# Performance work log

Hardware: AMD Instinct MI355X
Metric: run time of the kernel (lower is better)

Reference implementation:

```python
import jax, jax.numpy as jnp
import numpy as np


def setup_inputs() -> dict:
    key = jax.random.key(0)
    k1, k2, k3 = jax.random.split(key, 3)
    B, T, C, H, W = 4, 1024, 64, 8, 8
    E = C * H * W  # 4096 == embed_dim
    x = jax.random.normal(k1, (B, T, C, H, W), dtype=jnp.float32)
    Wqkv = jax.random.normal(k2, (E, 3 * E), dtype=jnp.float32) * (E ** -0.5)
    Wout = jax.random.normal(k3, (E, E), dtype=jnp.float32) * (E ** -0.5)
    bout = jnp.zeros((E,), dtype=jnp.float32)
    return {"x": x, "Wqkv": Wqkv, "Wout": Wout, "bout": bout}


def reference(x, Wqkv, Wout, bout):
    B, T, C, H, W = x.shape
    E = C * H * W
    heads = 8
    dh = E // heads
    # NOTE: original scales by embed_dim**-0.5, NOT head_dim**-0.5
    scale = E ** -0.5

    xf = x.reshape(B, T, E)                      # [B,T,E]
    qkv = xf @ Wqkv                              # [B,T,3E]
    q, k, v = jnp.split(qkv, 3, axis=-1)
    q = q.reshape(B, T, heads, dh)
    k = k.reshape(B, T, heads, dh)
    v = v.reshape(B, T, heads, dh)

    scores = jnp.einsum('bthd,bshd->bhts', q, k) * scale  # [B,h,T,T]
    attn = jax.nn.softmax(scores, axis=-1)
    out = jnp.einsum('bhts,bshd->bthd', attn, v)           # [B,T,h,dh]
    out = out.reshape(B, T, E) @ Wout + bout               # [B,T,E]
    return out.reshape(B, T, C, H, W)
```

## Files before the change

### kernel.cpp

```cpp
#include <hip/hip_runtime.h>
#include <hip/hip_bf16.h>

typedef __attribute__((ext_vector_type(8))) __bf16 bf16x8;
typedef __attribute__((ext_vector_type(4))) __bf16 bf16x4;
typedef __attribute__((ext_vector_type(4))) float f32x4;
typedef __attribute__((ext_vector_type(4))) int i32x4;

#define MFMA16(a, b, c) __builtin_amdgcn_mfma_f32_16x16x32_bf16((a), (b), (c), 0, 0, 0)
#define MFMAI8(a, b, c) __builtin_amdgcn_mfma_i32_16x16x64_i8((a), (b), (c), 0, 0, 0)

__global__ __launch_bounds__(256) void k_quantX(const float* __restrict__ x,
                                                __bf16* __restrict__ xb,
                                                char* __restrict__ xi8,
                                                float* __restrict__ sa) {
  int row = blockIdx.x, tid = threadIdx.x;
  const float* src = x + (size_t)row * 4096 + tid * 16;
  float arr[16];
#pragma unroll
  for (int j = 0; j < 4; ++j) {
    float4 v = ((const float4*)src)[j];
    arr[j * 4 + 0] = v.x; arr[j * 4 + 1] = v.y;
    arr[j * 4 + 2] = v.z; arr[j * 4 + 3] = v.w;
  }
  float m = 0.f;
#pragma unroll
  for (int e = 0; e < 16; ++e) m = fmaxf(m, fabsf(arr[e]));
#pragma unroll
  for (int off = 32; off; off >>= 1) m = fmaxf(m, __shfl_xor(m, off, 64));
  __shared__ float wmx[4];
  if ((tid & 63) == 0) wmx[tid >> 6] = m;
  __syncthreads();
  m = fmaxf(fmaxf(wmx[0], wmx[1]), fmaxf(wmx[2], wmx[3]));
  m = fmaxf(m, 1e-20f);
  float inv = 127.f / m;
  __bf16* db = xb + (size_t)row * 4096 + tid * 16;
#pragma unroll
  for (int j = 0; j < 2; ++j) {
    bf16x8 o;
#pragma unroll
    for (int e = 0; e < 8; ++e) o[e] = (__bf16)arr[j * 8 + e];
    *(bf16x8*)(db + j * 8) = o;
  }
  int pk[4];
#pragma unroll
  for (int j = 0; j < 4; ++j) {
    int w = 0;
#pragma unroll
    for (int e = 0; e < 4; ++e) {
      int q = (int)__builtin_rintf(arr[j * 4 + e] * inv);
      q = q < -127 ? -127 : (q > 127 ? 127 : q);
      w |= (q & 255) << (e * 8);
    }
    pk[j] = w;
  }
  int4 pv; pv.x = pk[0]; pv.y = pk[1]; pv.z = pk[2]; pv.w = pk[3];
  *(int4*)(xi8 + (size_t)row * 4096 + tid * 16) = pv;
  if (tid == 0) sa[row] = m / 127.f;
}

__global__ __launch_bounds__(256) void k_quantW(const __bf16* __restrict__ wT,
                                                char* __restrict__ wi8,
                                                float* __restrict__ sb) {
  int row = blockIdx.x, tid = threadIdx.x;
  const __bf16* src = wT + (size_t)row * 4096 + tid * 16;
  float arr[16];
#pragma unroll
  for (int j = 0; j < 2; ++j) {
    bf16x8 v = *(const bf16x8*)(src + j * 8);
#pragma unroll
    for (int e = 0; e < 8; ++e) arr[j * 8 + e] = (float)v[e];
  }
  float m = 0.f;
#pragma unroll
  for (int e = 0; e < 16; ++e) m = fmaxf(m, fabsf(arr[e]));
#pragma unroll
  for (int off = 32; off; off >>= 1) m = fmaxf(m, __shfl_xor(m, off, 64));
  __shared__ float wmx[4];
  if ((tid & 63) == 0) wmx[tid >> 6] = m;
  __syncthreads();
  m = fmaxf(fmaxf(wmx[0], wmx[1]), fmaxf(wmx[2], wmx[3]));
  m = fmaxf(m, 1e-20f);
  float inv = 127.f / m;
  int pk[4];
#pragma unroll
  for (int j = 0; j < 4; ++j) {
    int w = 0;
#pragma unroll
    for (int e = 0; e < 4; ++e) {
      int q = (int)__builtin_rintf(arr[j * 4 + e] * inv);
      q = q < -127 ? -127 : (q > 127 ? 127 : q);
      w |= (q & 255) << (e * 8);
    }
    pk[j] = w;
  }
  int4 pv; pv.x = pk[0]; pv.y = pk[1]; pv.z = pk[2]; pv.w = pk[3];
  *(int4*)(wi8 + (size_t)row * 4096 + tid * 16) = pv;
  if (tid == 0) sb[row] = m / 127.f;
}

__global__ __launch_bounds__(256) void k_prep(const float* __restrict__ Wqkv,
                                              __bf16* __restrict__ wT) {
  __shared__ float tl[64][68];
  int id = blockIdx.x, tid = threadIdx.x;
  int c0 = (id % 192) * 64, r0 = (id / 192) * 64;
  const int R = 4096, C = 12288;
#pragma unroll
  for (int j = 0; j < 4; ++j) {
    int idx = j * 256 + tid;
    int row = idx >> 4, q4 = (idx & 15) * 4;
    float4 v = *(const float4*)(Wqkv + (size_t)(r0 + row) * C + c0 + q4);
    tl[row][q4 + 0] = v.x; tl[row][q4 + 1] = v.y;
    tl[row][q4 + 2] = v.z; tl[row][q4 + 3] = v.w;
  }
  __syncthreads();
#pragma unroll
  for (int j = 0; j < 2; ++j) {
    int idx = j * 256 + tid;
    int orow = idx >> 3, ch = (idx & 7) * 8;
    bf16x8 pk;
#pragma unroll
    for (int e = 0; e < 8; ++e) pk[e] = (__bf16)tl[ch + e][orow];
    *(bf16x8*)(wT + (size_t)(c0 + orow) * R + r0 + ch) = pk;
  }
}

__global__ __launch_bounds__(256) void k_post1(const __bf16* __restrict__ qkv,
                                               __bf16* __restrict__ vt,
                                               const float* __restrict__ Wout,
                                               __bf16* __restrict__ woT) {
  __shared__ float tlf[64][68];
  __shared__ __bf16 tlh[64][72];
  int id = blockIdx.x, tid = threadIdx.x;
  if (id < 4096) {
    int bx = id & 7, by = (id >> 3) & 15, p = id >> 7;
    int b = p >> 3, h = p & 7;
    int d0 = bx * 64, s0 = by * 64;
    const __bf16* src = qkv + (size_t)b * 1024 * 12288 + 8192 + h * 512;
#pragma unroll
    for (int j = 0; j < 2; ++j) {
      int idx = j * 256 + tid;
      int row = idx >> 3, ch = (idx & 7) * 8;
      bf16x8 v = *(const bf16x8*)(src + (size_t)(s0 + row) * 12288 + d0 + ch);
#pragma unroll
      for (int e = 0; e < 8; ++e) tlh[row][ch + e] = v[e];
    }
    __syncthreads();
#pragma unroll
    for (int j = 0; j < 2; ++j) {
      int idx = j * 256 + tid;
      int orow = idx >> 3, ch = (idx & 7) * 8;
      bf16x8 pk;
#pragma unroll
      for (int e = 0; e < 8; ++e) pk[e] = tlh[ch + e][orow];
      *(bf16x8*)(vt + (size_t)p * 524288 + (size_t)(d0 + orow) * 1024 + s0 + ch) = pk;
    }
    return;
  }
  int t = id - 4096;
  int c0 = (t & 63) * 64, r0 = (t >> 6) * 64;
  const int R = 4096, C = 4096;
#pragma unroll
  for (int j = 0; j < 4; ++j) {
    int idx = j * 256 + tid;
    int row = idx >> 4, q4 = (idx & 15) * 4;
    float4 v = *(const float4*)(Wout + (size_t)(r0 + row) * C + c0 + q4);
    tlf[row][q4 + 0] = v.x; tlf[row][q4 + 1] = v.y;
    tlf[row][q4 + 2] = v.z; tlf[row][q4 + 3] = v.w;
  }
  __syncthreads();
#pragma unroll
  for (int j = 0; j < 2; ++j) {
    int idx = j * 256 + tid;
    int orow = idx >> 3, ch = (idx & 7) * 8;
    bf16x8 pk;
#pragma unroll
    for (int e = 0; e < 8; ++e) pk[e] = (__bf16)tlf[ch + e][orow];
    *(bf16x8*)(woT + (size_t)(c0 + orow) * R + r0 + ch) = pk;
  }
}

#define BARRIER() __builtin_amdgcn_s_barrier()
#define SCHED0() __builtin_amdgcn_sched_barrier(0)
#define VMC8() asm volatile("s_waitcnt vmcnt(8)" ::: "memory")
#define VMC4() asm volatile("s_waitcnt vmcnt(4)" ::: "memory")
#define LGKM(N)                                                   \
  do {                                                            \
    asm volatile("s_waitcnt lgkmcnt(" #N ")" ::: "memory");       \
    __builtin_amdgcn_sched_barrier(0);                            \
  } while (0)

#define LDA(AF, buf, mh)                                                      \
  do {                                                                        \
    _Pragma("unroll") for (int mi = 0; mi < 4; ++mi) {                        \
      int r = wm * 64 + mi * 16 + r16;                                        \
      _Pragma("unroll") for (int ks = 0; ks < 2; ++ks) {                      \
        int gg = ks * 4 + g;                                                  \
        AF[mi][ks] = *(const bf16x8*)(ldsB + (buf)*32768 + (mh)*16384 +       \
                                      r * 128 + ((gg ^ (r & 7)) << 4));       \
      }                                                                       \
    }                                                                         \
  } while (0)

#define LDB(BQ, buf, nh)                                                      \
  do {                                                                        \
    _Pragma("unroll") for (int ni = 0; ni < 2; ++ni) {                        \
      int r = wn * 32 + ni * 16 + r16;                                        \
      _Pragma("unroll") for (int ks = 0; ks < 2; ++ks) {                      \
        int gg = ks * 4 + g;                                                  \
        BQ[ni][ks] = *(const bf16x8*)(ldsB + 65536 + (buf)*32768 +            \
                                      (nh)*16384 + r * 128 +                  \
                                      ((gg ^ (r & 7)) << 4));                 \
      }                                                                       \
    }                                                                         \
  } while (0)

#define QUAD(AF, mh, nh, BQ)                                                  \
  do {                                                                        \
    __builtin_amdgcn_s_setprio(1);                                            \
    _Pragma("unroll") for (int ks = 0; ks < 2; ++ks)                          \
        _Pragma("unroll") for (int mi = 0; mi < 4; ++mi)                      \
            _Pragma("unroll") for (int ni = 0; ni < 2; ++ni)                  \
                acc[(mh)*4 + mi][(nh)*2 + ni] =                               \
                    MFMA16(AF[mi][ks], BQ[ni][ks],                            \
                           acc[(mh)*4 + mi][(nh)*2 + ni]);                    \
    __builtin_amdgcn_s_setprio(0);                                            \
    __builtin_amdgcn_sched_barrier(0);                                        \
  } while (0)

#define STAGE_A(mh, tau)                                                      \
  do {                                                                        \
    int tc = (tau) < NT ? (tau) : NT - 1;                                     \
    char* dbase = ldsB + ((tau)&1) * 32768 + (mh)*16384;                      \
    _Pragma("unroll") for (int i = 0; i < 2; ++i)                             \
        __builtin_amdgcn_global_load_lds(                                     \
            (const __attribute__((address_space(1))) void*)(Ap +              \
                offA[i][mh] + tc * 64),                                       \
            (__attribute__((address_space(3))) void*)(dbase +                 \
                (i * 512 + w * 64) * 16), 16, 0, 0);                          \
  } while (0)

#define STAGE_B(nh, tau)                                                      \
  do {                                                                        \
    int tc = (tau) < NT ? (tau) : NT - 1;                                     \
    char* dbase = ldsB + 65536 + ((tau)&1) * 32768 + (nh)*16384;              \
    _Pragma("unroll") for (int i = 0; i < 2; ++i)                             \
        __builtin_amdgcn_global_load_lds(                                     \
            (const __attribute__((address_space(1))) void*)(Bp +              \
                offB[i][nh] + tc * 64),                                       \
            (__attribute__((address_space(3))) void*)(dbase +                 \
                (i * 512 + w * 64) * 16), 16, 0, 0);                          \
  } while (0)

#define STAGE4(tau)                                                           \
  do {                                                                        \
    STAGE_A(0, tau); STAGE_B(0, tau); STAGE_B(1, tau); STAGE_A(1, tau);       \
  } while (0)

#define TILE_LOOP()                                                           \
  STAGE4(0);                                                                  \
  STAGE4(1);                                                                  \
  for (int t = 0; t < NT; ++t) {                                              \
    int buf = t & 1;                                                          \
    VMC8();                                                                   \
    BARRIER();                                                                \
    LDA(af, buf, 0);                                                          \
    LDB(bq0, buf, 0);                                                         \
    SCHED0();                                                                 \
    LDB(bq1, buf, 1);                                                         \
    SCHED0();                                                                 \
    LDA(af2, buf, 1);                                                         \
    LGKM(12);                                                                 \
    QUAD(af, 0, 0, bq0);                                                      \
    LGKM(8);                                                                  \
    QUAD(af, 0, 1, bq1);                                                      \
    LGKM(0);                                                                  \
    BARRIER();                                                                \
    STAGE4(t + 2);                                                            \
    QUAD(af2, 1, 1, bq1);                                                     \
    QUAD(af2, 1, 0, bq0);                                                     \
  }

#define SETUP_OFFSETS()                                                       \
  int offA[2][2], offB[2][2];                                                 \
  _Pragma("unroll") for (int i = 0; i < 2; ++i) {                             \
    int c = i * 512 + tid;                                                    \
    int r = c >> 3, slot = c & 7;                                             \
    int colsw = (slot ^ (r & 7)) << 3;                                        \
    _Pragma("unroll") for (int h = 0; h < 2; ++h) {                           \
      int RA = (r >> 6) * 128 + h * 64 + (r & 63);                            \
      int RB = (r >> 5) * 64 + h * 32 + (r & 31);                             \
      offA[i][h] = RA * lda + colsw;                                          \
      offB[i][h] = RB * ldb + colsw;                                          \
    }                                                                         \
  }

template <int MODE>
__global__ __launch_bounds__(512, 2) void k_gemm8(
    const __bf16* __restrict__ Abase, const __bf16* __restrict__ Bbase,
    void* __restrict__ Cout, const float* __restrict__ aux,
    int lda, int ldb, int N, int K) {
  __shared__ __align__(128) __bf16 lds[65536];
  char* ldsB = (char*)lds;
  int tid = threadIdx.x;
  int w = tid >> 6, lane = tid & 63;
  int r16 = lane & 15, g = lane >> 4;
  int wm = w >> 2, wn = w & 3;

  int bx, by, z = blockIdx.z;
  if (MODE <= 1) {
    int gx = gridDim.x, gy = gridDim.y;
    int RX = gx >> 2, RY = gy >> 1;
    int orig = blockIdx.y * gx + blockIdx.x;
    int xcd = orig & 7, idx = orig >> 3;
    int lbx = idx / RY, lby = idx - lbx * RY;
    bx = (xcd & 3) * RX + lbx;
    by = (xcd >> 2) * RY + lby;
  } else if (MODE == 2) {
    int i = blockIdx.z * 16 + blockIdx.y * 4 + blockIdx.x;
    z = (i & 7) | (((i >> 7) & 3) << 3);
    int qt = (i >> 3) & 15;
    by = qt >> 2; bx = qt & 3;
  } else {
    int i = blockIdx.z * 8 + blockIdx.y * 2 + blockIdx.x;
    z = (i & 7) | (((i >> 6) & 3) << 3);
    int qt = (i >> 3) & 7;
    by = qt >> 1; bx = qt & 1;
  }
  int m0 = by * 256, n0 = bx * 256;

  const __bf16 *Ap, *Bp;
  if (MODE == 2) {
    int b = z >> 3, h = z & 7;
    Ap = Abase + (size_t)b * 1024 * 12288 + h * 512;
    Bp = Abase + (size_t)b * 1024 * 12288 + 4096 + h * 512;
  } else if (MODE == 3) {
    Ap = Abase + (size_t)z * 1048576;
    Bp = Bbase + (size_t)z * 524288;
  } else {
    Ap = Abase; Bp = Bbase;
  }
  Ap += (size_t)m0 * lda;
  Bp += (size_t)n0 * ldb;
  SETUP_OFFSETS()

  int NT = K >> 6;
  f32x4 acc[8][4];
#pragma unroll
  for (int a = 0; a < 8; ++a)
#pragma unroll
    for (int bq = 0; bq < 4; ++bq) acc[a][bq] = f32x4{0.f, 0.f, 0.f, 0.f};
  bf16x8 af[4][2], af2[4][2], bq0[2][2], bq1[2][2];

  TILE_LOOP()

  if (MODE == 2) {
    asm volatile("s_waitcnt vmcnt(0)" ::: "memory");
    __syncthreads();
    float* Lbuf = (float*)ldsB;
#pragma unroll
    for (int mig = 0; mig < 8; ++mig) {
#pragma unroll
      for (int ii = 0; ii < 4; ++ii) {
        int row = m0 + wm * 128 + mig * 16 + g * 4 + ii;
        float s = 0.f;
#pragma unroll
        for (int nig = 0; nig < 4; ++nig) {
          int col = n0 + wn * 64 + nig * 16 + r16;
          float e = __expf(acc[mig][nig][ii] * 0.015625f);
          ((__bf16*)Cout)[(size_t)z * 1048576 + (size_t)row * 1024 + col] =
              (__bf16)e;
          s += e;
        }
        s += __shfl_xor(s, 1, 64);
        s += __shfl_xor(s, 2, 64);
        s += __shfl_xor(s, 4, 64);
        s += __shfl_xor(s, 8, 64);
        if (r16 == 0)
          Lbuf[(wm * 4 + wn) * 128 + mig * 16 + g * 4 + ii] = s;
      }
    }
    __syncthreads();
    if (tid < 256) {
      int wmi = tid >> 7, rl = tid & 127;
      const float* base = Lbuf + wmi * 512;
      float s = base[rl] + base[128 + rl] + base[256 + rl] + base[384 + rl];
      ((float*)aux)[z * 4096 + bx * 1024 + m0 + tid] = s;
    }
    return;
  }

#pragma unroll
  for (int mig = 0; mig < 8; ++mig) {
#pragma unroll
    for (int ii = 0; ii < 4; ++ii) {
      int row = m0 + wm * 128 + mig * 16 + g * 4 + ii;
      float lval = 0.f;
      if (MODE == 3)
        lval = aux[z * 4096 + row] + aux[z * 4096 + 1024 + row] +
               aux[z * 4096 + 2048 + row] + aux[z * 4096 + 3072 + row];
#pragma unroll
      for (int nig = 0; nig < 4; ++nig) {
        int col = n0 + wn * 64 + nig * 16 + r16;
        float v = acc[mig][nig][ii];
        if (MODE == 0) {
          ((__bf16*)Cout)[(size_t)row * N + col] = (__bf16)v;
        } else if (MODE == 1) {
          ((float*)Cout)[(size_t)row * N + col] = v + aux[col];
        } else if (MODE == 3) {
          ((__bf16*)Cout)[(size_t)((z >> 3) * 1024 + row) * 4096 +
                          (z & 7) * 512 + col] = (__bf16)(v / lval);
        }
      }
    }
  }
}

#define I8_SWZ(r) (((r) & 3) ^ (((r) >> 2) & 3))

#define I8_STAGE(tau)                                                         \
  do {                                                                        \
    int tc = (tau) < NT ? (tau) : NT - 1;                                     \
    char* da = ldsB + ((tau)&1) * 32768;                                      \
    _Pragma("unroll") for (int h = 0; h < 2; ++h) {                           \
      __builtin_amdgcn_global_load_lds(                                       \
          (const __attribute__((address_space(1))) void*)(Ap + offA[h] +      \
                                                          tc * 64),           \
          (__attribute__((address_space(3))) void*)(da + h * 8192 +           \
              w * 1024), 16, 0, 0);                                           \
      __builtin_amdgcn_global_load_lds(                                       \
          (const __attribute__((address_space(1))) void*)(Bp + offB[h] +      \
                                                          tc * 64),           \
          (__attribute__((address_space(3))) void*)(da + 16384 + h * 8192 +   \
              w * 1024), 16, 0, 0);                                           \
    }                                                                         \
  } while (0)

#define I8_QUAD(MIBASE)                                                       \
  do {                                                                        \
    __builtin_amdgcn_s_setprio(1);                                            \
    _Pragma("unroll") for (int mi = 0; mi < 4; ++mi)                          \
        _Pragma("unroll") for (int ni = 0; ni < 4; ++ni)                      \
            acc[(MIBASE) + mi][ni] = MFMAI8(af[mi], bq[ni],                   \
                                            acc[(MIBASE) + mi][ni]);          \
    __builtin_amdgcn_s_setprio(0);                                            \
    __builtin_amdgcn_sched_barrier(0);                                        \
  } while (0)

__global__ __launch_bounds__(512, 2) void k_gemm_i8(
    const char* __restrict__ Abase, const char* __restrict__ Bbase,
    __bf16* __restrict__ Cout, const float* __restrict__ sa,
    const float* __restrict__ sb) {
  __shared__ __align__(128) char ldsB[65536];
  const int lda = 4096, ldb = 4096, NT = 64;
  int tid = threadIdx.x;
  int w = tid >> 6, lane = tid & 63;
  int r16 = lane & 15, g = lane >> 4;
  int wm = w >> 2, wn = w & 3;

  int gx = gridDim.x, gy = gridDim.y;
  int RX = gx >> 2, RY = gy >> 1;
  int orig = blockIdx.y * gx + blockIdx.x;
  int xcd = orig & 7, idx = orig >> 3;
  int lbx = idx / RY, lby = idx - lbx * RY;
  int bx = (xcd & 3) * RX + lbx;
  int by = (xcd >> 2) * RY + lby;
  int m0 = by * 256, n0 = bx * 256;

  const char* Ap = Abase + (size_t)m0 * lda;
  const char* Bp = Bbase + (size_t)n0 * ldb;

  int offA[2], offB[2];
  {
    int rl = tid >> 2, slot = tid & 3;
    int slotg = (slot ^ I8_SWZ(rl)) << 4;
#pragma unroll
    for (int h = 0; h < 2; ++h) {
      offA[h] = (h * 128 + rl) * lda + slotg;
      offB[h] = (h * 128 + rl) * ldb + slotg;
    }
  }

  i32x4 acc[8][4];
#pragma unroll
  for (int a = 0; a < 8; ++a)
#pragma unroll
    for (int b = 0; b < 4; ++b) acc[a][b] = i32x4{0, 0, 0, 0};
  i32x4 af[4], af2[4], bq[4];

  I8_STAGE(0);
  I8_STAGE(1);
  for (int t = 0; t < NT; ++t) {
    int buf = t & 1;
    VMC4();
    BARRIER();
    {
      char* bbase = ldsB + buf * 32768 + 16384 + (wn >> 1) * 8192;
#pragma unroll
      for (int ni = 0; ni < 4; ++ni) {
        int rb = (wn & 1) * 64 + ni * 16 + r16;
        bq[ni] = *(const i32x4*)(bbase + rb * 64 + ((g ^ I8_SWZ(rb)) << 4));
      }
    }
    SCHED0();
    {
      char* abase = ldsB + buf * 32768 + wm * 8192;
#pragma unroll
      for (int mi = 0; mi < 4; ++mi) {
        int r = mi * 16 + r16;
        af[mi] = *(const i32x4*)(abase + r * 64 + ((g ^ I8_SWZ(r)) << 4));
      }
      SCHED0();
#pragma unroll
      for (int mi = 0; mi < 4; ++mi) {
        int r = 64 + mi * 16 + r16;
        af2[mi] = *(const i32x4*)(abase + r * 64 + ((g ^ I8_SWZ(r)) << 4));
      }
    }
    LGKM(4);
    I8_QUAD(0);
    LGKM(0);
    BARRIER();
    I8_STAGE(t + 2);
#pragma unroll
    for (int mi = 0; mi < 4; ++mi) af[mi] = af2[mi];
    I8_QUAD(4);
  }

#pragma unroll
  for (int mig = 0; mig < 8; ++mig) {
#pragma unroll
    for (int ii = 0; ii < 4; ++ii) {
      int row = m0 + wm * 128 + ((mig >> 2) * 64) + (mig & 3) * 16 + g * 4 + ii;
      float sav = sa[row];
#pragma unroll
      for (int nig = 0; nig < 4; ++nig) {
        int col = n0 + wn * 64 + nig * 16 + r16;
        float v = (float)acc[mig][nig][ii] * sav * sb[col];
        Cout[(size_t)row * 12288 + col] = (__bf16)v;
      }
    }
  }
}

extern "C" void kernel_launch(void* const* d_in, const int* in_sizes, int n_in,
                              void* d_out, int out_size, void* d_ws, size_t ws_size,
                              hipStream_t stream) {
  const float* x = (const float*)d_in[0];
  const float* Wqkv = (const float*)d_in[1];
  const float* Wout = (const float*)d_in[2];
  const float* bout = (const float*)d_in[3];
  float* out = (float*)d_out;
  char* ws = (char*)d_ws;

  __bf16* xb = (__bf16*)(ws);
  __bf16* wT = (__bf16*)(ws + 33554432);
  __bf16* P = (__bf16*)(ws + 33554432);
  __bf16* woT = (__bf16*)(ws + 33554432 + 67108864);
  __bf16* qkv = (__bf16*)(ws + 134217728);
  char* wi8 = (char*)(ws + 234881024);
  __bf16* vt = (__bf16*)(ws + 234881024);

  char* xi8 = (char*)d_out;
  float* sa = (float*)((char*)d_out + 16777216);
  float* sb = (float*)((char*)d_out + 16777216 + 65536);
  float* Lpart = (float*)((char*)d_out + 33554432);

  k_quantX<<<4096, 256, 0, stream>>>(x, xb, xi8, sa);
  k_prep<<<12288, 256, 0, stream>>>(Wqkv, wT);
  k_quantW<<<8192, 256, 0, stream>>>(wT, wi8, sb);
  k_gemm_i8<<<dim3(32, 16), 512, 0, stream>>>(xi8, wi8, qkv, sa, sb);
  k_gemm8<0><<<dim3(16, 16), 512, 0, stream>>>(
      xb, wT + (size_t)8192 * 4096, qkv + 8192, nullptr, 4096, 4096, 12288, 4096);
  k_post1<<<8192, 256, 0, stream>>>(qkv, vt, Wout, woT);
  k_gemm8<2><<<dim3(4, 4, 32), 512, 0, stream>>>(qkv, qkv, P, Lpart, 12288, 12288, 1024, 512);
  k_gemm8<3><<<dim3(2, 4, 32), 512, 0, stream>>>(P, vt, xb, Lpart, 1024, 1024, 512, 1024);
  k_gemm8<1><<<dim3(16, 16), 512, 0, stream>>>(xb, woT, out, bout, 4096, 4096, 4096, 4096);
}
```

Baseline: 584.5 us.

## Triple-buffer int8 GEMM LDS pipeline and merge quantX with weight transpose kernel

The int8 QKV GEMM goes from two LDS stages to three (96KB of LDS), prefetching two tiles ahead and waiting on vmcnt(8) instead of vmcnt(4), so global loads have more time to land. The x quantization kernel and the Wqkv transpose/convert kernel are merged into one launch that picks its path by block index, removing a launch boundary. The larger LDS footprint caps occupancy at one block per CU, and the merged kernel's shared tile also serves as the reduction scratch.

```diff
diff --git a/kernel.cpp b/kernel.cpp
--- a/kernel.cpp
+++ b/kernel.cpp
@@ -9,53 +9,81 @@
 #define MFMA16(a, b, c) __builtin_amdgcn_mfma_f32_16x16x32_bf16((a), (b), (c), 0, 0, 0)
 #define MFMAI8(a, b, c) __builtin_amdgcn_mfma_i32_16x16x64_i8((a), (b), (c), 0, 0, 0)
 
-__global__ __launch_bounds__(256) void k_quantX(const float* __restrict__ x,
-                                                __bf16* __restrict__ xb,
-                                                char* __restrict__ xi8,
-                                                float* __restrict__ sa) {
-  int row = blockIdx.x, tid = threadIdx.x;
-  const float* src = x + (size_t)row * 4096 + tid * 16;
-  float arr[16];
+__global__ __launch_bounds__(256) void k_prep(const float* __restrict__ x,
+                                              __bf16* __restrict__ xb,
+                                              char* __restrict__ xi8,
+                                              float* __restrict__ sa,
+                                              const float* __restrict__ Wqkv,
+                                              __bf16* __restrict__ wT) {
+  __shared__ float tl[64][68];
+  int id = blockIdx.x, tid = threadIdx.x;
+  if (id < 4096) {
+    int row = id;
+    const float* src = x + (size_t)row * 4096 + tid * 16;
+    float arr[16];
+#pragma unroll
+    for (int j = 0; j < 4; ++j) {
+      float4 v = ((const float4*)src)[j];
+      arr[j * 4 + 0] = v.x; arr[j * 4 + 1] = v.y;
+      arr[j * 4 + 2] = v.z; arr[j * 4 + 3] = v.w;
+    }
+    float m = 0.f;
+#pragma unroll
+    for (int e = 0; e < 16; ++e) m = fmaxf(m, fabsf(arr[e]));
+#pragma unroll
+    for (int off = 32; off; off >>= 1) m = fmaxf(m, __shfl_xor(m, off, 64));
+    float* wmx = &tl[0][0];
+    if ((tid & 63) == 0) wmx[tid >> 6] = m;
+    __syncthreads();
+    m = fmaxf(fmaxf(wmx[0], wmx[1]), fmaxf(wmx[2], wmx[3]));
+    m = fmaxf(m, 1e-20f);
+    float inv = 127.f / m;
+    __bf16* db = xb + (size_t)row * 4096 + tid * 16;
+#pragma unroll
+    for (int j = 0; j < 2; ++j) {
+      bf16x8 o;
+#pragma unroll
+      for (int e = 0; e < 8; ++e) o[e] = (__bf16)arr[j * 8 + e];
+      *(bf16x8*)(db + j * 8) = o;
+    }
+    int pk[4];
+#pragma unroll
+    for (int j = 0; j < 4; ++j) {
+      int wv = 0;
+#pragma unroll
+      for (int e = 0; e < 4; ++e) {
+        int q = (int)__builtin_rintf(arr[j * 4 + e] * inv);
+        q = q < -127 ? -127 : (q > 127 ? 127 : q);
+        wv |= (q & 255) << (e * 8);
+      }
+      pk[j] = wv;
+    }
+    int4 pv; pv.x = pk[0]; pv.y = pk[1]; pv.z = pk[2]; pv.w = pk[3];
+    *(int4*)(xi8 + (size_t)row * 4096 + tid * 16) = pv;
+    if (tid == 0) sa[row] = m / 127.f;
+    return;
+  }
+  int t = id - 4096;
+  int c0 = (t % 192) * 64, r0 = (t / 192) * 64;
+  const int R = 4096, C = 12288;
 #pragma unroll
   for (int j = 0; j < 4; ++j) {
-    float4 v = ((const float4*)src)[j];
-    arr[j * 4 + 0] = v.x; arr[j * 4 + 1] = v.y;
-    arr[j * 4 + 2] = v.z; arr[j * 4 + 3] = v.w;
-  }
-  float m = 0.f;
-#pragma unroll
-  for (int e = 0; e < 16; ++e) m = fmaxf(m, fabsf(arr[e]));
-#pragma unroll
-  for (int off = 32; off; off >>= 1) m = fmaxf(m, __shfl_xor(m, off, 64));
-  __shared__ float wmx[4];
-  if ((tid & 63) == 0) wmx[tid >> 6] = m;
+    int idx = j * 256 + tid;
+    int row = idx >> 4, q4 = (idx & 15) * 4;
+    float4 v = *(const float4*)(Wqkv + (size_t)(r0 + row) * C + c0 + q4);
+    tl[row][q4 + 0] = v.x; tl[row][q4 + 1] = v.y;
+    tl[row][q4 + 2] = v.z; tl[row][q4 + 3] = v.w;
+  }
   __syncthreads();
-  m = fmaxf(fmaxf(wmx[0], wmx[1]), fmaxf(wmx[2], wmx[3]));
-  m = fmaxf(m, 1e-20f);
-  float inv = 127.f / m;
-  __bf16* db = xb + (size_t)row * 4096 + tid * 16;
 #pragma unroll
   for (int j = 0; j < 2; ++j) {
-    bf16x8 o;
-#pragma unroll
-    for (int e = 0; e < 8; ++e) o[e] = (__bf16)arr[j * 8 + e];
-    *(bf16x8*)(db + j * 8) = o;
-  }
-  int pk[4];
-#pragma unroll
-  for (int j = 0; j < 4; ++j) {
-    int w = 0;
-#pragma unroll
-    for (int e = 0; e < 4; ++e) {
-      int q = (int)__builtin_rintf(arr[j * 4 + e] * inv);
-      q = q < -127 ? -127 : (q > 127 ? 127 : q);
-      w |= (q & 255) << (e * 8);
-    }
-    pk[j] = w;
-  }
-  int4 pv; pv.x = pk[0]; pv.y = pk[1]; pv.z = pk[2]; pv.w = pk[3];
-  *(int4*)(xi8 + (size_t)row * 4096 + tid * 16) = pv;
-  if (tid == 0) sa[row] = m / 127.f;
+    int idx = j * 256 + tid;
+    int orow = idx >> 3, ch = (idx & 7) * 8;
+    bf16x8 pk;
+#pragma unroll
+    for (int e = 0; e < 8; ++e) pk[e] = (__bf16)tl[ch + e][orow];
+    *(bf16x8*)(wT + (size_t)(c0 + orow) * R + r0 + ch) = pk;
+  }
 }
 
 __global__ __launch_bounds__(256) void k_quantW(const __bf16* __restrict__ wT,
@@ -96,32 +124,6 @@
   int4 pv; pv.x = pk[0]; pv.y = pk[1]; pv.z = pk[2]; pv.w = pk[3];
   *(int4*)(wi8 + (size_t)row * 4096 + tid * 16) = pv;
   if (tid == 0) sb[row] = m / 127.f;
-}
-
-__global__ __launch_bounds__(256) void k_prep(const float* __restrict__ Wqkv,
-                                              __bf16* __restrict__ wT) {
-  __shared__ float tl[64][68];
-  int id = blockIdx.x, tid = threadIdx.x;
-  int c0 = (id % 192) * 64, r0 = (id / 192) * 64;
-  const int R = 4096, C = 12288;
-#pragma unroll
-  for (int j = 0; j < 4; ++j) {
-    int idx = j * 256 + tid;
-    int row = idx >> 4, q4 = (idx & 15) * 4;
-    float4 v = *(const float4*)(Wqkv + (size_t)(r0 + row) * C + c0 + q4);
-    tl[row][q4 + 0] = v.x; tl[row][q4 + 1] = v.y;
-    tl[row][q4 + 2] = v.z; tl[row][q4 + 3] = v.w;
-  }
-  __syncthreads();
-#pragma unroll
-  for (int j = 0; j < 2; ++j) {
-    int idx = j * 256 + tid;
-    int orow = idx >> 3, ch = (idx & 7) * 8;
-    bf16x8 pk;
-#pragma unroll
-    for (int e = 0; e < 8; ++e) pk[e] = (__bf16)tl[ch + e][orow];
-    *(bf16x8*)(wT + (size_t)(c0 + orow) * R + r0 + ch) = pk;
-  }
 }
 
 __global__ __launch_bounds__(256) void k_post1(const __bf16* __restrict__ qkv,
@@ -182,7 +184,6 @@
 #define BARRIER() __builtin_amdgcn_s_barrier()
 #define SCHED0() __builtin_amdgcn_sched_barrier(0)
 #define VMC8() asm volatile("s_waitcnt vmcnt(8)" ::: "memory")
-#define VMC4() asm volatile("s_waitcnt vmcnt(4)" ::: "memory")
 #define LGKM(N)                                                   \
   do {                                                            \
     asm volatile("s_waitcnt lgkmcnt(" #N ")" ::: "memory");       \
@@ -417,10 +418,10 @@
 
 #define I8_SWZ(r) (((r) & 3) ^ (((r) >> 2) & 3))
 
-#define I8_STAGE(tau)                                                         \
+#define I8_STAGE(tau, base)                                                   \
   do {                                                                        \
     int tc = (tau) < NT ? (tau) : NT - 1;                                     \
-    char* da = ldsB + ((tau)&1) * 32768;                                      \
+    char* da = (base);                                                        \
     _Pragma("unroll") for (int h = 0; h < 2; ++h) {                           \
       __builtin_amdgcn_global_load_lds(                                       \
           (const __attribute__((address_space(1))) void*)(Ap + offA[h] +      \
@@ -450,7 +451,7 @@
     const char* __restrict__ Abase, const char* __restrict__ Bbase,
     __bf16* __restrict__ Cout, const float* __restrict__ sa,
     const float* __restrict__ sb) {
-  __shared__ __align__(128) char ldsB[65536];
+  __shared__ __align__(128) char ldsB[98304];
   const int lda = 4096, ldb = 4096, NT = 64;
   int tid = threadIdx.x;
   int w = tid >> 6, lane = tid & 63;
@@ -487,14 +488,16 @@
     for (int b = 0; b < 4; ++b) acc[a][b] = i32x4{0, 0, 0, 0};
   i32x4 af[4], af2[4], bq[4];
 
-  I8_STAGE(0);
-  I8_STAGE(1);
+  I8_STAGE(0, ldsB);
+  I8_STAGE(1, ldsB + 32768);
+  I8_STAGE(2, ldsB + 65536);
+  int bufo = 0;
   for (int t = 0; t < NT; ++t) {
-    int buf = t & 1;
-    VMC4();
+    char* base = ldsB + bufo * 32768;
+    VMC8();
     BARRIER();
     {
-      char* bbase = ldsB + buf * 32768 + 16384 + (wn >> 1) * 8192;
+      char* bbase = base + 16384 + (wn >> 1) * 8192;
 #pragma unroll
       for (int ni = 0; ni < 4; ++ni) {
         int rb = (wn & 1) * 64 + ni * 16 + r16;
@@ -503,7 +506,7 @@
     }
     SCHED0();
     {
-      char* abase = ldsB + buf * 32768 + wm * 8192;
+      char* abase = base + wm * 8192;
 #pragma unroll
       for (int mi = 0; mi < 4; ++mi) {
         int r = mi * 16 + r16;
@@ -520,10 +523,11 @@
     I8_QUAD(0);
     LGKM(0);
     BARRIER();
-    I8_STAGE(t + 2);
+    I8_STAGE(t + 3, base);
 #pragma unroll
     for (int mi = 0; mi < 4; ++mi) af[mi] = af2[mi];
     I8_QUAD(4);
+    bufo = (bufo == 2) ? 0 : bufo + 1;
   }
 
 #pragma unroll
@@ -565,8 +569,7 @@
   float* sb = (float*)((char*)d_out + 16777216 + 65536);
   float* Lpart = (float*)((char*)d_out + 33554432);
 
-  k_quantX<<<4096, 256, 0, stream>>>(x, xb, xi8, sa);
-  k_prep<<<12288, 256, 0, stream>>>(Wqkv, wT);
+  k_prep<<<16384, 256, 0, stream>>>(x, xb, xi8, sa, Wqkv, wT);
   k_quantW<<<8192, 256, 0, stream>>>(wT, wi8, sb);
   k_gemm_i8<<<dim3(32, 16), 512, 0, stream>>>(xi8, wi8, qkv, sa, sb);
   k_gemm8<0><<<dim3(16, 16), 512, 0, stream>>>(
```

New measurement: 580.5 us. About the same (-0.7%).
